# Optimization experiments

Hardware: AMD Instinct MI355X
Metric: run time of the kernel (lower is better)

## Reference

```python
import jax, jax.numpy as jnp
import numpy as np

NUM_PAGES = 1048576
TOKENS_PER_PAGE = 32
SLOTS = 256
MAX_PAGES_PER_SLOT = 4096
MAX_SEQ = 65536  # <= max_pages_per_slot*tokens_per_page/2, leaves room to grow


def setup_inputs() -> dict:
    key = jax.random.key(0)
    k1, = jax.random.split(key, 1)
    # random current sequence lengths per slot (some may be 0 / inactive)
    seq = jax.random.randint(k1, (SLOTS,), 0, MAX_SEQ).astype(jnp.int32)
    npu = (seq + TOKENS_PER_PAGE - 1) // TOKENS_PER_PAGE  # ceil-div pages used
    cols = jnp.arange(MAX_PAGES_PER_SLOT, dtype=jnp.int32)
    # give slot i the disjoint page-id range [1 + i*2048, ...); valid since
    # max pages/slot here = ceil(65535/32) = 2048 and 1+255*2048+2047 < NUM_PAGES
    pm = jnp.where(
        cols[None, :] < npu[:, None],
        1 + jnp.arange(SLOTS, dtype=jnp.int32)[:, None] * 2048 + cols[None, :],
        -1,
    ).astype(jnp.int32)
    # mark exactly the mapped pages as in-use (index 0 used as a safe dump slot)
    safe_idx = jnp.where(pm > -1, pm, 0)
    vals = (pm > -1).astype(jnp.int32)
    page_status = jnp.zeros((NUM_PAGES,), jnp.int32).at[safe_idx].max(vals)
    page_status = page_status.at[0].set(0)
    current_page = jnp.where(
        npu > 0,
        jnp.take_along_axis(pm, jnp.maximum(npu - 1, 0)[:, None], axis=1)[:, 0],
        -1,
    ).astype(jnp.int32)
    cpp = jnp.where(seq == 0, 0, (seq - 1) % TOKENS_PER_PAGE).astype(jnp.int32)
    return {
        "page_status": page_status,
        "page_map": pm,
        "sequence_lengths": seq,
        "num_pages_used": npu.astype(jnp.int32),
        "current_page": current_page,
        "current_page_position": cpp,
    }


def _find_next_free_page(page_status):
    # matches PageManager.find_next_free_page: first free index in [1, N), else 0
    free = jnp.where(page_status[1:] == 0, size=1, fill_value=-1)[0] + 1
    return free[0].astype(jnp.int32)


def reference(page_status, page_map, sequence_lengths, num_pages_used,
              current_page, current_page_position):
    """Faithful port of PageManager.reserve_decode_step_pages (autoregressive step)."""
    tpp = TOKENS_PER_PAGE
    new_seq = sequence_lengths + jnp.where(current_page == -1, 0, 1).astype(jnp.int32)
    new_npu = (new_seq + tpp - 1) // tpp
    new_cpp = jnp.where(new_seq == 0, 0, (new_seq - 1) % tpp).astype(jnp.int32)

    def step(carry, i):
        ps, pm, cp = carry
        needs_new_page = new_npu[i] > num_pages_used[i]
        nfp = jax.lax.cond(
            needs_new_page,
            lambda: _find_next_free_page(ps),
            lambda: jnp.int32(-1),
        )
        ps = jax.lax.cond(needs_new_page, lambda x: x.at[nfp].set(1), lambda x: x, ps)
        pm = jax.lax.cond(
            needs_new_page,
            lambda x: x.at[i, num_pages_used[i]].set(nfp),
            lambda x: x,
            pm,
        )
        cp = jax.lax.cond(needs_new_page, lambda x: x.at[i].set(nfp), lambda x: x, cp)
        return (ps, pm, cp), None

    (ps, pm, cp), _ = jax.lax.scan(
        step, (page_status, page_map, current_page), jnp.arange(SLOTS, dtype=jnp.int32)
    )
    # PageState fields in declaration order
    return (ps, pm, new_seq, new_npu.astype(jnp.int32), cp, new_cpp)
```

## Files before the change

kernel.cpp:

```cpp
#include <hip/hip_runtime.h>

#define NUM_PAGES 1048576
#define TPP 32
#define SLOTS 256
#define MPPS 4096
#define NBLK 1024
#define NTHR 256

#define ELEM(v, j) ((j) == 0 ? (v).x : (j) == 1 ? (v).y : (j) == 2 ? (v).z : (v).w)

__global__ __launch_bounds__(NTHR) void fused(
    const int* __restrict__ ps, const int* __restrict__ pm,
    const int* __restrict__ seq, const int* __restrict__ npu,
    const int* __restrict__ cp, int* __restrict__ out)
{
    const int t = threadIdx.x, b = blockIdx.x;
    const int lane = t & 63, wave = t >> 6;

    int* out_ps  = out;
    int* out_pm  = out + NUM_PAGES;
    int* out_seq = out + 2 * NUM_PAGES;
    int* out_npu = out_seq + SLOTS;
    int* out_cp  = out_npu + SLOTS;
    int* out_cpp = out_cp + SLOTS;

    __shared__ int s_free[SLOTS];
    __shared__ int s_info[SLOTS];
    __shared__ int s_col[SLOTS];
    __shared__ int s_cpo[SLOTS];
    __shared__ int s_K, s_fe;

    const int4* ps4 = reinterpret_cast<const int4*>(ps);
    const int gi = b * NTHR + t;

    if (wave == 0) {
        const int4 sq4 = reinterpret_cast<const int4*>(seq)[lane];
        const int4 cq4 = reinterpret_cast<const int4*>(cp)[lane];
        const int4 nu4 = reinterpret_cast<const int4*>(npu)[lane];
        int4 pc[8];
        #pragma unroll
        for (int r = 0; r < 8; ++r) pc[r] = ps4[r * 64 + lane];
        const int4 pv = ps4[gi];
        const int4 mv = reinterpret_cast<const int4*>(pm)[gi];

        int ns0, ns1, ns2, ns3, nn0, nn1, nn2, nn3, nb = 0;
        ns0 = sq4.x + (cq4.x != -1); nn0 = (ns0 + TPP - 1) / TPP; if (nn0 > nu4.x) nb |= 1;
        ns1 = sq4.y + (cq4.y != -1); nn1 = (ns1 + TPP - 1) / TPP; if (nn1 > nu4.y) nb |= 2;
        ns2 = sq4.z + (cq4.z != -1); nn2 = (ns2 + TPP - 1) / TPP; if (nn2 > nu4.z) nb |= 4;
        ns3 = sq4.w + (cq4.w != -1); nn3 = (ns3 + TPP - 1) / TPP; if (nn3 > nu4.w) nb |= 8;

        if (b == 0) {
            int4 o;
            o.x = ns0; o.y = ns1; o.z = ns2; o.w = ns3;
            reinterpret_cast<int4*>(out_seq)[lane] = o;
            o.x = nn0; o.y = nn1; o.z = nn2; o.w = nn3;
            reinterpret_cast<int4*>(out_npu)[lane] = o;
            o.x = (ns0 == 0) ? 0 : ((ns0 - 1) & (TPP - 1));
            o.y = (ns1 == 0) ? 0 : ((ns1 - 1) & (TPP - 1));
            o.z = (ns2 == 0) ? 0 : ((ns2 - 1) & (TPP - 1));
            o.w = (ns3 == 0) ? 0 : ((ns3 - 1) & (TPP - 1));
            reinterpret_cast<int4*>(out_cpp)[lane] = o;
        }

        int cnt = __popc(nb), x = cnt;
        #pragma unroll
        for (int o = 1; o < 64; o <<= 1) { int y = __shfl_up(x, o); if (lane >= o) x += y; }
        const int K = __shfl(x, 63);
        const int base_r = x - cnt;
        int4 iv;
        iv.x = (nb & 1) ? base_r : -1;
        iv.y = (nb & 2) ? base_r + __popc(nb & 1) : -1;
        iv.z = (nb & 4) ? base_r + __popc(nb & 3) : -1;
        iv.w = (nb & 8) ? base_r + __popc(nb & 7) : -1;
        reinterpret_cast<int4*>(s_info)[lane] = iv;
        reinterpret_cast<int4*>(s_col)[lane]  = nu4;
        reinterpret_cast<int4*>(s_cpo)[lane]  = cq4;

        auto doRound = [&](int4 v, int pagebase, int sf) -> int {
            int m = ((v.x == 0) ? 1 : 0) | ((v.y == 0) ? 2 : 0) |
                    ((v.z == 0) ? 4 : 0) | ((v.w == 0) ? 8 : 0);
            if (pagebase == 0 && lane == 0) m &= ~1;
            int q = __popc(m), xx = q;
            #pragma unroll
            for (int o = 1; o < 64; o <<= 1) { int y = __shfl_up(xx, o); if (lane >= o) xx += y; }
            int pos = sf + xx - q;
            #pragma unroll
            for (int j = 0; j < 4; ++j) if (m & (1 << j)) {
                int p = pos + __popc(m & ((1 << j) - 1));
                if (p < K) s_free[p] = pagebase + lane * 4 + j;
            }
            return sf + __shfl(xx, 63);
        };

        int sf = 0;
        #pragma unroll
        for (int r = 0; r < 8; ++r)
            if (sf < K) sf = doRound(pc[r], r * 256, sf);
        for (int pb = 2048; pb < NUM_PAGES && sf < K; pb += 256)
            sf = doRound(ps4[(pb >> 2) + lane], pb, sf);

        if (lane == 0) { s_K = K; s_fe = (sf < K) ? sf : K; }

        reinterpret_cast<int4*>(out_ps)[gi] = pv;
        reinterpret_cast<int4*>(out_pm)[gi] = mv;
    } else {
        const int4 pv = ps4[gi];
        const int4 mv = reinterpret_cast<const int4*>(pm)[gi];
        reinterpret_cast<int4*>(out_ps)[gi] = pv;
        reinterpret_cast<int4*>(out_pm)[gi] = mv;
    }

    __syncthreads();

    const int K = s_K, fe = s_fe;

    if (t < K) {
        int f = (t < fe) ? s_free[t] : 0;
        if ((f >> 10) == b) out_ps[f] = 1;
    }
    if (t == 64) {
        int slot = b >> 2, info = s_info[slot];
        if (info >= 0) {
            int col = s_col[slot];
            if ((col >> 10) == (b & 3))
                out_pm[slot * MPPS + col] = (info < fe) ? s_free[info] : 0;
        }
    }
    if (b == 0) {
        int info = s_info[t];
        out_cp[t] = (info >= 0) ? ((info < fe) ? s_free[info] : 0) : s_cpo[t];
    }
}

extern "C" void kernel_launch(void* const* d_in, const int* in_sizes, int n_in,
                              void* d_out, int out_size, void* d_ws, size_t ws_size,
                              hipStream_t stream)
{
    const int* page_status = (const int*)d_in[0];
    const int* page_map    = (const int*)d_in[1];
    const int* seq         = (const int*)d_in[2];
    const int* npu         = (const int*)d_in[3];
    const int* cp          = (const int*)d_in[4];

    fused<<<NBLK, NTHR, 0, stream>>>(
        page_status, page_map, seq, npu, cp, (int*)d_out);
}
```

Baseline: 11.08 us.

## Replicate free-page scan in every wave to drop block barrier and scattered writes

Every wave now runs the prefix-sum scan for free pages itself. Each thread works out which of its own page_status and page_map elements need patching and folds those into the single vectorised copy store, which removes the __syncthreads and the separate scattered global writes. The scan also uses a three-deep register prefetch of page_status rows. The cost is redundant scan work and extra loads in all 4096 waves, plus per-round ballot logic. A barrier is kept only in block 0, where it is needed for the current_page output.

```diff
diff --git a/kernel.cpp b/kernel.cpp
--- a/kernel.cpp
+++ b/kernel.cpp
@@ -6,8 +6,8 @@
 #define MPPS 4096
 #define NBLK 1024
 #define NTHR 256
+#define NR4 (NUM_PAGES / 1024)
 
-#define ELEM(v, j) ((j) == 0 ? (v).x : (j) == 1 ? (v).y : (j) == 2 ? (v).z : (v).w)
 
 __global__ __launch_bounds__(NTHR) void fused(
     const int* __restrict__ ps, const int* __restrict__ pm,
@@ -25,110 +25,126 @@
     int* out_cpp = out_cp + SLOTS;
 
     __shared__ int s_free[SLOTS];
-    __shared__ int s_info[SLOTS];
-    __shared__ int s_col[SLOTS];
+    __shared__ int s_rank[SLOTS];
     __shared__ int s_cpo[SLOTS];
-    __shared__ int s_K, s_fe;
 
     const int4* ps4 = reinterpret_cast<const int4*>(ps);
     const int gi = b * NTHR + t;
+    const int my_round = 4 * b + wave;
 
-    if (wave == 0) {
-        const int4 sq4 = reinterpret_cast<const int4*>(seq)[lane];
-        const int4 cq4 = reinterpret_cast<const int4*>(cp)[lane];
-        const int4 nu4 = reinterpret_cast<const int4*>(npu)[lane];
-        int4 pc[8];
-        #pragma unroll
-        for (int r = 0; r < 8; ++r) pc[r] = ps4[r * 64 + lane];
-        const int4 pv = ps4[gi];
-        const int4 mv = reinterpret_cast<const int4*>(pm)[gi];
+    const int4 sq4 = reinterpret_cast<const int4*>(seq)[lane];
+    const int4 cq4 = reinterpret_cast<const int4*>(cp)[lane];
+    const int4 nu4 = reinterpret_cast<const int4*>(npu)[lane];
+    int4 A = ps4[lane];
+    int4 B = ps4[64 + lane];
+    int4 C = ps4[128 + lane];
+    const int4 pv = ps4[gi];
+    const int4 mv = reinterpret_cast<const int4*>(pm)[gi];
 
-        int ns0, ns1, ns2, ns3, nn0, nn1, nn2, nn3, nb = 0;
-        ns0 = sq4.x + (cq4.x != -1); nn0 = (ns0 + TPP - 1) / TPP; if (nn0 > nu4.x) nb |= 1;
-        ns1 = sq4.y + (cq4.y != -1); nn1 = (ns1 + TPP - 1) / TPP; if (nn1 > nu4.y) nb |= 2;
-        ns2 = sq4.z + (cq4.z != -1); nn2 = (ns2 + TPP - 1) / TPP; if (nn2 > nu4.z) nb |= 4;
-        ns3 = sq4.w + (cq4.w != -1); nn3 = (ns3 + TPP - 1) / TPP; if (nn3 > nu4.w) nb |= 8;
+    int ns0 = sq4.x + (cq4.x != -1), nn0 = (ns0 + TPP - 1) >> 5;
+    int ns1 = sq4.y + (cq4.y != -1), nn1 = (ns1 + TPP - 1) >> 5;
+    int ns2 = sq4.z + (cq4.z != -1), nn2 = (ns2 + TPP - 1) >> 5;
+    int ns3 = sq4.w + (cq4.w != -1), nn3 = (ns3 + TPP - 1) >> 5;
+    int nb = (nn0 > nu4.x ? 1 : 0) | (nn1 > nu4.y ? 2 : 0) |
+             (nn2 > nu4.z ? 4 : 0) | (nn3 > nu4.w ? 8 : 0);
 
-        if (b == 0) {
-            int4 o;
-            o.x = ns0; o.y = ns1; o.z = ns2; o.w = ns3;
-            reinterpret_cast<int4*>(out_seq)[lane] = o;
-            o.x = nn0; o.y = nn1; o.z = nn2; o.w = nn3;
-            reinterpret_cast<int4*>(out_npu)[lane] = o;
-            o.x = (ns0 == 0) ? 0 : ((ns0 - 1) & (TPP - 1));
-            o.y = (ns1 == 0) ? 0 : ((ns1 - 1) & (TPP - 1));
-            o.z = (ns2 == 0) ? 0 : ((ns2 - 1) & (TPP - 1));
-            o.w = (ns3 == 0) ? 0 : ((ns3 - 1) & (TPP - 1));
-            reinterpret_cast<int4*>(out_cpp)[lane] = o;
-        }
+    int cnt = __popc(nb), x = cnt;
+    #pragma unroll
+    for (int o = 1; o < 64; o <<= 1) { int y = __shfl_up(x, o); if (lane >= o) x += y; }
+    const int K = __shfl(x, 63);
+    const int base_r = x - cnt;
+    const int iv0 = (nb & 1) ? base_r : -1;
+    const int iv1 = (nb & 2) ? base_r + (nb & 1) : -1;
+    const int iv2 = (nb & 4) ? base_r + __popc(nb & 3) : -1;
+    const int iv3 = (nb & 8) ? base_r + __popc(nb & 7) : -1;
 
-        int cnt = __popc(nb), x = cnt;
-        #pragma unroll
-        for (int o = 1; o < 64; o <<= 1) { int y = __shfl_up(x, o); if (lane >= o) x += y; }
-        const int K = __shfl(x, 63);
-        const int base_r = x - cnt;
-        int4 iv;
-        iv.x = (nb & 1) ? base_r : -1;
-        iv.y = (nb & 2) ? base_r + __popc(nb & 1) : -1;
-        iv.z = (nb & 4) ? base_r + __popc(nb & 3) : -1;
-        iv.w = (nb & 8) ? base_r + __popc(nb & 7) : -1;
-        reinterpret_cast<int4*>(s_info)[lane] = iv;
-        reinterpret_cast<int4*>(s_col)[lane]  = nu4;
-        reinterpret_cast<int4*>(s_cpo)[lane]  = cq4;
-
-        auto doRound = [&](int4 v, int pagebase, int sf) -> int {
-            int m = ((v.x == 0) ? 1 : 0) | ((v.y == 0) ? 2 : 0) |
-                    ((v.z == 0) ? 4 : 0) | ((v.w == 0) ? 8 : 0);
-            if (pagebase == 0 && lane == 0) m &= ~1;
-            int q = __popc(m), xx = q;
-            #pragma unroll
-            for (int o = 1; o < 64; o <<= 1) { int y = __shfl_up(xx, o); if (lane >= o) xx += y; }
-            int pos = sf + xx - q;
-            #pragma unroll
-            for (int j = 0; j < 4; ++j) if (m & (1 << j)) {
-                int p = pos + __popc(m & ((1 << j) - 1));
-                if (p < K) s_free[p] = pagebase + lane * 4 + j;
-            }
-            return sf + __shfl(xx, 63);
-        };
-
-        int sf = 0;
-        #pragma unroll
-        for (int r = 0; r < 8; ++r)
-            if (sf < K) sf = doRound(pc[r], r * 256, sf);
-        for (int pb = 2048; pb < NUM_PAGES && sf < K; pb += 256)
-            sf = doRound(ps4[(pb >> 2) + lane], pb, sf);
-
-        if (lane == 0) { s_K = K; s_fe = (sf < K) ? sf : K; }
-
-        reinterpret_cast<int4*>(out_ps)[gi] = pv;
-        reinterpret_cast<int4*>(out_pm)[gi] = mv;
-    } else {
-        const int4 pv = ps4[gi];
-        const int4 mv = reinterpret_cast<const int4*>(pm)[gi];
-        reinterpret_cast<int4*>(out_ps)[gi] = pv;
-        reinterpret_cast<int4*>(out_pm)[gi] = mv;
+    if (b == 0 && wave == 0) {
+        int4 o;
+        o.x = ns0; o.y = ns1; o.z = ns2; o.w = ns3;
+        reinterpret_cast<int4*>(out_seq)[lane] = o;
+        o.x = nn0; o.y = nn1; o.z = nn2; o.w = nn3;
+        reinterpret_cast<int4*>(out_npu)[lane] = o;
+        o.x = ns0 ? ((ns0 - 1) & 31) : 0;
+        o.y = ns1 ? ((ns1 - 1) & 31) : 0;
+        o.z = ns2 ? ((ns2 - 1) & 31) : 0;
+        o.w = ns3 ? ((ns3 - 1) & 31) : 0;
+        reinterpret_cast<int4*>(out_cpp)[lane] = o;
+        o.x = iv0; o.y = iv1; o.z = iv2; o.w = iv3;
+        reinterpret_cast<int4*>(s_rank)[lane] = o;
+        reinterpret_cast<int4*>(s_cpo)[lane] = cq4;
     }
 
-    __syncthreads();
+    const int slot_b = b >> 2;
+    const int src_lane = slot_b >> 2;
+    const int jb = slot_b & 3;
+    int my_iv = (jb == 0) ? iv0 : (jb == 1) ? iv1 : (jb == 2) ? iv2 : iv3;
+    int my_nu = (jb == 0) ? nu4.x : (jb == 1) ? nu4.y : (jb == 2) ? nu4.z : nu4.w;
+    const int tr    = __shfl(my_iv, src_lane);
+    const int col_b = __shfl(my_nu, src_lane);
 
-    const int K = s_K, fe = s_fe;
+    int sf = 0, pmask = 0, nfp_pm = -1, r = 0;
+    while (sf < K && r < NR4) {
+        int4 v = A; A = B; B = C;
+        C = (r + 3 < NR4) ? ps4[(r + 3) * 64 + lane] : make_int4(1, 1, 1, 1);
+        int m = ((v.x == 0) ? 1 : 0) | ((v.y == 0) ? 2 : 0) |
+                ((v.z == 0) ? 4 : 0) | ((v.w == 0) ? 8 : 0);
+        if (r == 0 && lane == 0) m &= ~1;
+        int q = __popc(m), xx = q;
+        #pragma unroll
+        for (int o = 1; o < 64; o <<= 1) { int y = __shfl_up(xx, o); if (lane >= o) xx += y; }
+        int pos = sf + xx - q;
+        int p0 = pos;
+        int p1 = pos + (m & 1);
+        int p2 = pos + __popc(m & 3);
+        int p3 = pos + __popc(m & 7);
+        int pg = r * 256 + lane * 4;
+        if (r == my_round) {
+            if ((m & 1) && p0 < K) pmask |= 1;
+            if ((m & 2) && p1 < K) pmask |= 2;
+            if ((m & 4) && p2 < K) pmask |= 4;
+            if ((m & 8) && p3 < K) pmask |= 8;
+        }
+        if (b == 0) {
+            if ((m & 1) && p0 < K) s_free[p0] = pg;
+            if ((m & 2) && p1 < K) s_free[p1] = pg + 1;
+            if ((m & 4) && p2 < K) s_free[p2] = pg + 2;
+            if ((m & 8) && p3 < K) s_free[p3] = pg + 3;
+        }
+        if (tr >= 0 && nfp_pm < 0) {
+            int fl = -1;
+            if ((m & 1) && p0 == tr) fl = pg;
+            if ((m & 2) && p1 == tr) fl = pg + 1;
+            if ((m & 4) && p2 == tr) fl = pg + 2;
+            if ((m & 8) && p3 == tr) fl = pg + 3;
+            unsigned long long bb = __ballot(fl >= 0);
+            if (bb) nfp_pm = __shfl(fl, __ffsll(bb) - 1);
+        }
+        sf += __shfl(xx, 63);
+        ++r;
+    }
+    const int fe = (sf < K) ? sf : K;
 
-    if (t < K) {
-        int f = (t < fe) ? s_free[t] : 0;
-        if ((f >> 10) == b) out_ps[f] = 1;
+    int4 opv = pv, omv = mv;
+    if (gi == 0 && fe < K) pmask |= 1;
+    if (pmask & 1) opv.x = 1;
+    if (pmask & 2) opv.y = 1;
+    if (pmask & 4) opv.z = 1;
+    if (pmask & 8) opv.w = 1;
+    if (tr >= 0) {
+        int nfp = (tr < fe) ? nfp_pm : 0;
+        int d = col_b - ((b & 3) << 10) - (t << 2);
+        if (d == 0) omv.x = nfp;
+        else if (d == 1) omv.y = nfp;
+        else if (d == 2) omv.z = nfp;
+        else if (d == 3) omv.w = nfp;
     }
-    if (t == 64) {
-        int slot = b >> 2, info = s_info[slot];
-        if (info >= 0) {
-            int col = s_col[slot];
-            if ((col >> 10) == (b & 3))
-                out_pm[slot * MPPS + col] = (info < fe) ? s_free[info] : 0;
-        }
-    }
+    reinterpret_cast<int4*>(out_ps)[gi] = opv;
+    reinterpret_cast<int4*>(out_pm)[gi] = omv;
+
     if (b == 0) {
-        int info = s_info[t];
-        out_cp[t] = (info >= 0) ? ((info < fe) ? s_free[info] : 0) : s_cpo[t];
+        __syncthreads();
+        int rk = s_rank[t];
+        out_cp[t] = (rk >= 0) ? ((rk < fe) ? s_free[rk] : 0) : s_cpo[t];
     }
 }
 
```

Measured after the change: 12.42 us. 12.1% more time.
